# Performance work log

Hardware: AMD Instinct MI355X
Metric: run time of the kernel (lower is better)

## Reference

```python
import jax, jax.numpy as jnp
import numpy as np

B = 4; C_IN = 3; HW = 224
D_MODEL = 384; D_INNER = 768; D_STATE = 16; DT_RANK = 24; D_CONV = 4
N_LAYERS = 4; NUM_CLASSES = 1000
EPS = 1e-5


def setup_inputs() -> dict:
    key = jax.random.key(0)
    ks = jax.random.split(key, 12)
    def rn(k, shape, scale=0.02):
        return jax.random.normal(k, shape, jnp.float32) * scale
    inp = {}
    inp["x"] = jax.random.normal(ks[0], (B, C_IN, HW, HW), jnp.float32)
    inp["patch_w"] = rn(ks[1], (D_MODEL, C_IN, 4, 4))
    inp["patch_b"] = jnp.zeros((D_MODEL,), jnp.float32)
    inp["in_proj_w"] = rn(ks[2], (N_LAYERS, 2 * D_INNER, D_MODEL))
    inp["conv_w"] = rn(ks[3], (N_LAYERS, D_INNER, 1, D_CONV))
    inp["conv_b"] = jnp.zeros((N_LAYERS, D_INNER), jnp.float32)
    inp["x_proj_w"] = rn(ks[4], (N_LAYERS, DT_RANK + 2 * D_STATE, D_INNER))
    inp["dt_proj_w"] = rn(ks[5], (N_LAYERS, D_INNER, DT_RANK))
    inp["dt_proj_b"] = rn(ks[6], (N_LAYERS, D_INNER), 0.1)
    A = jnp.tile(jnp.arange(1, D_STATE + 1, dtype=jnp.float32)[None, :], (D_INNER, 1))
    inp["A_log"] = jnp.tile(jnp.log(A)[None], (N_LAYERS, 1, 1))
    inp["Dp"] = jnp.ones((N_LAYERS, D_INNER), jnp.float32)
    inp["out_proj_w"] = rn(ks[7], (N_LAYERS, D_MODEL, D_INNER))
    inp["norm_w"] = jnp.ones((D_MODEL,), jnp.float32)
    inp["head_w"] = rn(ks[8], (NUM_CLASSES, D_MODEL))
    inp["head_b"] = jnp.zeros((NUM_CLASSES,), jnp.float32)
    return inp


def selective_scan(u, delta, A, Bm, Cm, Dv):
    # u, delta: [b,l,d]; A: [d,n]; Bm, Cm: [b,l,n]; Dv: [d]
    dA = jnp.exp(delta[..., None] * A)                 # [b,l,d,n]
    dBu = (delta * u)[..., None] * Bm[:, :, None, :]   # [b,l,d,n]

    def step(h, inp):
        a, bu, c = inp
        h = a * h + bu                                  # [b,d,n]
        y = jnp.einsum('bdn,bn->bd', h, c)
        return h, y

    h0 = jnp.zeros((u.shape[0], u.shape[2], A.shape[1]), u.dtype)
    xs = (jnp.swapaxes(dA, 0, 1), jnp.swapaxes(dBu, 0, 1), jnp.swapaxes(Cm, 0, 1))
    _, ys = jax.lax.scan(step, h0, xs)                  # ys: [l,b,d]
    y = jnp.swapaxes(ys, 0, 1)                          # [b,l,d]
    return y + u * Dv


def mamba_block(x, p):
    xr = x @ p['in_proj_w'].T                           # [b,l,2*d_inner]
    xc, res = jnp.split(xr, 2, axis=-1)
    # depthwise causal conv1d (left pad d_conv-1 == pad both + truncate right)
    xt = jnp.swapaxes(xc, 1, 2)                         # [b,d_inner,l]
    xt = jax.lax.conv_general_dilated(
        xt, p['conv_w'], (1,), [(D_CONV - 1, 0)],
        feature_group_count=D_INNER,
        dimension_numbers=('NCH', 'OIH', 'NCH')) + p['conv_b'][None, :, None]
    xc = jax.nn.silu(jnp.swapaxes(xt, 1, 2))
    # S6
    dbl = xc @ p['x_proj_w'].T                          # [b,l,dt_rank+2n]
    dt, Bm, Cm = jnp.split(dbl, [DT_RANK, DT_RANK + D_STATE], axis=-1)
    delta = jax.nn.softplus(dt @ p['dt_proj_w'].T + p['dt_proj_b'])
    y = selective_scan(xc, delta, -jnp.exp(p['A_log']), Bm, Cm, p['Dp'])
    y = y * jax.nn.silu(res)
    return y @ p['out_proj_w'].T


def reference(x, patch_w, patch_b, in_proj_w, conv_w, conv_b, x_proj_w,
              dt_proj_w, dt_proj_b, A_log, Dp, out_proj_w, norm_w, head_w, head_b):
    h = jax.lax.conv_general_dilated(
        x, patch_w, (4, 4), 'VALID',
        dimension_numbers=('NCHW', 'OIHW', 'NCHW')) + patch_b[None, :, None, None]
    b, d, hh, ww = h.shape
    t = jnp.transpose(h.reshape(b, d, hh * ww), (0, 2, 1))  # [b,l,d_model]
    layer_params = dict(in_proj_w=in_proj_w, conv_w=conv_w, conv_b=conv_b,
                        x_proj_w=x_proj_w, dt_proj_w=dt_proj_w, dt_proj_b=dt_proj_b,
                        A_log=A_log, Dp=Dp, out_proj_w=out_proj_w)
    for i in range(N_LAYERS):
        p = {k: v[i] for k, v in layer_params.items()}
        t = t + mamba_block(t, p)
    rms = jnp.sqrt(jnp.mean(t * t, axis=-1, keepdims=True) + EPS)
    t = t / rms * norm_w
    pooled = t.mean(axis=1)
    return pooled @ head_w.T + head_b
```

## Files before the change

kernel.cpp:

```cpp
#include <hip/hip_runtime.h>
#include <math.h>


namespace {
constexpr int NB = 4;
constexpr int SL = 3136;
constexpr int DM = 384;
constexpr int DI = 768;
constexpr int DSN = 16;
constexpr int DR = 24;
constexpr int NLAYER = 4;
constexpr int NCLS = 1000;
constexpr int XPN = DR + 2 * DSN;
constexpr int NCHAIN = NB * DI;
constexpr int PTOK = 32;
}

typedef float f32x4 __attribute__((ext_vector_type(4)));
typedef short short8 __attribute__((ext_vector_type(8)));
typedef short short4v __attribute__((ext_vector_type(4)));
typedef unsigned short us4 __attribute__((ext_vector_type(4)));

__device__ __forceinline__ float siluf(float x) { return x / (1.f + expf(-x)); }
__device__ __forceinline__ float softplusf(float x) {
  return fmaxf(x, 0.f) + log1pf(expf(-fabsf(x)));
}
__device__ __forceinline__ unsigned short cvt_bf(float f) {
  unsigned int x = __float_as_uint(f);
  unsigned int r = (x + 0x7fffu + ((x >> 16) & 1u)) >> 16;
  return (unsigned short)r;
}
__device__ __forceinline__ float bf2f(unsigned short v) {
  return __uint_as_float((unsigned int)v << 16);
}

__global__ __launch_bounds__(128) void k_patch(
    const float* __restrict__ x, const float* __restrict__ w,
    const float* __restrict__ bias, float* __restrict__ t,
    unsigned short* __restrict__ tb) {
  __shared__ float patch[PTOK][48];
  const int tid = threadIdx.x;
  const int m0 = blockIdx.x * PTOK;
  const int b = m0 / SL, lbase = m0 % SL;
#pragma unroll
  for (int i = 0; i < 3; ++i) {
    const int c = tid + i * 128;
    const int tok = c / 12, r = c % 12;
    const int ch = r >> 2, kh = r & 3;
    const int l = lbase + tok;
    const int hh = l / 56, ww = l % 56;
    const float4 v =
        *(const float4*)&x[((size_t)(b * 3 + ch) * 224 + (hh * 4 + kh)) * 224 + ww * 4];
    *(float4*)&patch[tok][ch * 16 + kh * 4] = v;
  }
  __syncthreads();
#pragma unroll 1
  for (int i = 0; i < 3; ++i) {
    const int dm = tid + i * 128;
    float4 wr[12];
    const float4* w4 = (const float4*)(w + (size_t)dm * 48);
#pragma unroll
    for (int q = 0; q < 12; ++q) wr[q] = w4[q];
    const float bv = bias[dm];
#pragma unroll 1
    for (int tok0 = 0; tok0 < PTOK; tok0 += 8) {
      float acc[8];
#pragma unroll
      for (int j = 0; j < 8; ++j) acc[j] = bv;
#pragma unroll
      for (int q = 0; q < 12; ++q) {
        const float4 wv = wr[q];
#pragma unroll
        for (int j = 0; j < 8; ++j) {
          const float4 pv = *(const float4*)&patch[tok0 + j][q * 4];
          acc[j] = fmaf(pv.x, wv.x, acc[j]);
          acc[j] = fmaf(pv.y, wv.y, acc[j]);
          acc[j] = fmaf(pv.z, wv.z, acc[j]);
          acc[j] = fmaf(pv.w, wv.w, acc[j]);
        }
      }
#pragma unroll
      for (int j = 0; j < 8; ++j) {
        const size_t o = ((size_t)(m0 + tok0 + j)) * DM + dm;
        t[o] = acc[j];
        tb[o] = cvt_bf(acc[j]);
      }
    }
  }
}

template <int BM, int BN, int MEPI, int NCAP, bool AT>
__global__ __launch_bounds__(256) void k_mgemm(
    const unsigned short* __restrict__ A, const unsigned short* __restrict__ Abf,
    const float* __restrict__ W, float* __restrict__ out,
    float* __restrict__ out2, unsigned short* __restrict__ outb, const int K) {
  constexpr int WM = BM / 2, WN = BN / 2, FM = WM / 16, FN = WN / 16;
  constexpr bool NMASK = (NCAP % BN) != 0;
  __shared__ unsigned short As[BM * 40];
  __shared__ unsigned short Bs[BN * 40];
  const int tid = threadIdx.x;
  const int lane = tid & 63, wave = tid >> 6;
  const int wm = wave >> 1, wn = wave & 1;
  const int m0 = blockIdx.x * BM, n0 = blockIdx.y * BN;
  const int r16 = lane & 15, kg = (lane >> 4) * 8;
  f32x4 acc[FM][FN] = {};
  const int nk = K >> 5;
  for (int kt = 0; kt < nk; ++kt) {
    const int k0 = kt << 5;
    if constexpr (AT) {
#pragma unroll
      for (int it = 0; it < BM / 64; ++it) {
        const int c = tid + 256 * it;
        const int kp = c & 15;
        const int lq = (c >> 4) * 4;
        const int mrow = m0 + lq;
        const int bb = mrow / SL;
        const size_t rowo = (size_t)(bb * K + k0 + 2 * kp) * SL + (mrow - bb * SL);
        const us4 v0 = *(const us4*)&Abf[rowo];
        const us4 v1 = *(const us4*)&Abf[rowo + SL];
#pragma unroll
        for (int e = 0; e < 4; ++e) {
          const unsigned int pk =
              (unsigned int)v0[e] | ((unsigned int)v1[e] << 16);
          *(unsigned int*)&As[(lq + e) * 40 + 2 * kp] = pk;
        }
      }
    } else {
#pragma unroll
      for (int it = 0; it < (BM * 4) / 256; ++it) {
        const int c = tid + 256 * it;
        const int row = c >> 2, ks = (c & 3) * 8;
        *(short8*)&As[row * 40 + ks] =
            *(const short8*)&A[(size_t)(m0 + row) * K + k0 + ks];
      }
    }
#pragma unroll
    for (int it = 0; it < (BN * 8) / 256; ++it) {
      const int c = tid + 256 * it;
      const int row = c >> 3, ks = (c & 7) * 4;
      float4 v = make_float4(0.f, 0.f, 0.f, 0.f);
      if (!NMASK || (n0 + row) < NCAP)
        v = *(const float4*)&W[(size_t)(n0 + row) * K + k0 + ks];
      short4v o4;
      o4[0] = (short)cvt_bf(v.x);
      o4[1] = (short)cvt_bf(v.y);
      o4[2] = (short)cvt_bf(v.z);
      o4[3] = (short)cvt_bf(v.w);
      *(short4v*)&Bs[row * 40 + ks] = o4;
    }
    __syncthreads();
    short8 af[FM], bfv[FN];
#pragma unroll
    for (int i = 0; i < FM; ++i)
      af[i] = *(const short8*)&As[(wm * WM + i * 16 + r16) * 40 + kg];
#pragma unroll
    for (int j = 0; j < FN; ++j)
      bfv[j] = *(const short8*)&Bs[(wn * WN + j * 16 + r16) * 40 + kg];
#pragma unroll
    for (int i = 0; i < FM; ++i)
#pragma unroll
      for (int j = 0; j < FN; ++j)
        acc[i][j] = __builtin_amdgcn_mfma_f32_16x16x32_bf16(af[i], bfv[j],
                                                            acc[i][j], 0, 0, 0);
    __syncthreads();
  }

#pragma unroll
  for (int i = 0; i < FM; ++i) {
#pragma unroll
    for (int j = 0; j < FN; ++j) {
      const int n = n0 + wn * WN + j * 16 + r16;
      const int mb = m0 + wm * WM + i * 16 + ((lane >> 4) << 2);
      f32x4 a = acc[i][j];
      if (MEPI == 0) {
        if (n < DR) {
#pragma unroll
          for (int r = 0; r < 4; ++r) out[(size_t)(mb + r) * DR + n] = a[r];
        } else if (n < NCAP) {
#pragma unroll
          for (int r = 0; r < 4; ++r) out2[(size_t)(mb + r) * 32 + (n - DR)] = a[r];
        }
      } else if (MEPI == 1) {
        unsigned short* base = (unsigned short*)out;
        int nn = n;
        if (n >= DI) { base = (unsigned short*)out2; nn = n - DI; }
        const int bb = mb / SL;
        const int ll = mb - bb * SL;
        us4 o4;
#pragma unroll
        for (int r = 0; r < 4; ++r) o4[r] = cvt_bf(a[r]);
        *(us4*)&base[((size_t)(bb * DI + nn)) * SL + ll] = o4;
      } else {
#pragma unroll
        for (int r = 0; r < 4; ++r) {
          const size_t off = (size_t)(mb + r) * DM + n;
          const float nv = out[off] + a[r];
          out[off] = nv;
          outb[off] = cvt_bf(nv);
        }
      }
    }
  }
}

template <int EPI, bool KTAIL, int NCAP>
__global__ __launch_bounds__(256) void k_gemm(
    const float* __restrict__ A, const float* __restrict__ W,
    const float* __restrict__ bias, float* __restrict__ out, int K, int lda) {
  __shared__ float sm[4352];
  const int tid = threadIdx.x;
  const int m0 = blockIdx.x * 64;
  const int n0 = blockIdx.y * 64;
  const int b = m0 / SL, l0 = m0 % SL;
  const int tm = tid >> 4, tn = tid & 15;
  float acc[4][4] = {};
  float* As = sm;
  float* Ws = sm + 16 * 68;

  const int nk = (K + 15) / 16;
  for (int kt = 0; kt < nk; ++kt) {
    const int k0 = kt * 16;
    {
      const int row = tid >> 2;
      const int kq = (tid & 3) * 4;
      const int kb = k0 + kq;
      float4 v = make_float4(0.f, 0.f, 0.f, 0.f);
      if (!KTAIL || kb < K) v = *(const float4*)&A[(size_t)(m0 + row) * lda + kb];
      As[(kq + 0) * 68 + row] = v.x;
      As[(kq + 1) * 68 + row] = v.y;
      As[(kq + 2) * 68 + row] = v.z;
      As[(kq + 3) * 68 + row] = v.w;
    }
    {
      const int row = tid >> 2;
      const int kq = (tid & 3) * 4;
      const int kb = k0 + kq;
      float4 v = make_float4(0.f, 0.f, 0.f, 0.f);
      const bool nok = (NCAP % 64 == 0) || (n0 + row < NCAP);
      if (nok && (!KTAIL || kb < K)) v = *(const float4*)&W[(size_t)(n0 + row) * K + kb];
      Ws[(kq + 0) * 68 + row] = v.x;
      Ws[(kq + 1) * 68 + row] = v.y;
      Ws[(kq + 2) * 68 + row] = v.z;
      Ws[(kq + 3) * 68 + row] = v.w;
    }
    __syncthreads();
#pragma unroll
    for (int kk = 0; kk < 16; ++kk) {
      const float4 av = *(const float4*)&As[kk * 68 + 4 * tm];
      const float4 wv = *(const float4*)&Ws[kk * 68 + 4 * tn];
      const float ax[4] = {av.x, av.y, av.z, av.w};
      const float wx[4] = {wv.x, wv.y, wv.z, wv.w};
#pragma unroll
      for (int i = 0; i < 4; ++i)
#pragma unroll
        for (int j = 0; j < 4; ++j) acc[i][j] = fmaf(ax[i], wx[j], acc[i][j]);
    }
    __syncthreads();
  }

#pragma unroll
  for (int j = 0; j < 4; ++j) {
    const int nn = 4 * tn + j;
#pragma unroll
    for (int i = 0; i < 4; ++i) {
      float v = acc[i][j];
      if (EPI == 2) v = softplusf(v + bias[n0 + nn]);
      sm[nn * 68 + 4 * tm + i] = v;
    }
  }
  __syncthreads();
  const int row = tid >> 2;
  const int seg = (tid & 3) * 16;
  const float* src = &sm[row * 68 + seg];
  float* dst = out + ((size_t)(b * DI + n0 + row)) * SL + l0 + seg;
#pragma unroll
  for (int q = 0; q < 4; ++q) {
    *(float4*)&dst[q * 4] = *(const float4*)&src[q * 4];
  }
}

__global__ void k_conv(const unsigned short* __restrict__ xcT,
                       const float* __restrict__ cw, const float* __restrict__ cb,
                       unsigned short* __restrict__ uT) {
  const size_t idx = (size_t)blockIdx.x * 256 + threadIdx.x;
  const int l4 = (int)(idx % (SL / 4)) * 4;
  const int bd = (int)(idx / (SL / 4));
  const int d = bd % DI;
  const unsigned short* row = xcT + (size_t)bd * SL;
  const float4 w = *(const float4*)&cw[d * 4];
  const us4 cu = *(const us4*)&row[l4];
  const float c0 = bf2f(cu[0]), c1 = bf2f(cu[1]), c2 = bf2f(cu[2]), c3 = bf2f(cu[3]);
  float p1 = 0.f, p2 = 0.f, p3 = 0.f;
  if (l4 > 0) {
    const us4 pv = *(const us4*)&row[l4 - 4];
    p1 = bf2f(pv[1]); p2 = bf2f(pv[2]); p3 = bf2f(pv[3]);
  }
  const float cbd = cb[d];
  float o0 = cbd + w.w * c0 + w.z * p3 + w.y * p2 + w.x * p1;
  float o1 = cbd + w.w * c1 + w.z * c0 + w.y * p3 + w.x * p2;
  float o2 = cbd + w.w * c2 + w.z * c1 + w.y * c0 + w.x * p3;
  float o3 = cbd + w.w * c3 + w.z * c2 + w.y * c1 + w.x * c0;
  us4 o4;
  o4[0] = cvt_bf(siluf(o0));
  o4[1] = cvt_bf(siluf(o1));
  o4[2] = cvt_bf(siluf(o2));
  o4[3] = cvt_bf(siluf(o3));
  *(us4*)&uT[(size_t)bd * SL + l4] = o4;
}

__global__ __launch_bounds__(256) void k_scanw(
    const float* __restrict__ deltaT, const unsigned short* __restrict__ uT,
    const float* __restrict__ BC, const unsigned short* __restrict__ resT,
    const float* __restrict__ A_log, const float* __restrict__ Dp,
    unsigned short* __restrict__ yT) {
  const int tid = threadIdx.x;
  const int lane = tid & 63, wv = tid >> 6;
  const int n = lane & 15, g = lane >> 4;
  const int chain = blockIdx.x * 4 + wv;
  const int b = chain / DI, d = chain % DI;
  const float a2 = -expf(A_log[d * DSN + n]) * 1.44269504088896341f;
  const float dp = Dp[d];
  const float* drow = deltaT + (size_t)chain * SL;
  const unsigned short* urow = uT + (size_t)chain * SL;
  const unsigned short* resr = resT + (size_t)chain * SL;
  const float* bcb = BC + (size_t)b * SL * 32;
  unsigned short* yr = yT + (size_t)chain * SL;
  float carry = 0.f;
  const bool b0 = n & 1, b1 = (n >> 1) & 1, b2 = (n >> 2) & 1, b3 = (n >> 3) & 1;

  for (int tb = 0; tb < SL; tb += 64) {
    const int l0 = tb + g * 16;
    float da[16], dbu[16];
    float h = 0.f, dsum = 0.f;
#pragma unroll
    for (int k = 0; k < 16; ++k) {
      const float dl = drow[l0 + k];
      const float ul = bf2f(urow[l0 + k]);
      const float Bv = bcb[(size_t)(l0 + k) * 32 + n];
      const float e = exp2f(dl * a2);
      da[k] = e;
      dbu[k] = dl * ul * Bv;
      h = fmaf(e, h, dbu[k]);
      dsum += dl;
    }
    float Aagg = exp2f(a2 * dsum);
    float Bagg = h;
#pragma unroll
    for (int off = 16; off <= 32; off <<= 1) {
      const float Ae = __shfl(Aagg, (lane - off) & 63);
      const float Be = __shfl(Bagg, (lane - off) & 63);
      if (lane >= off) {
        Bagg = fmaf(Aagg, Be, Bagg);
        Aagg *= Ae;
      }
    }
    const float Pa = __shfl(Aagg, (lane - 16) & 63);
    const float Pb = __shfl(Bagg, (lane - 16) & 63);
    const float hstart = (g == 0) ? carry : fmaf(Pa, carry, Pb);
    const float cA = __shfl(Aagg, 48 | n);
    const float cB = __shfl(Bagg, 48 | n);
    float p[16];
    h = hstart;
#pragma unroll
    for (int k = 0; k < 16; ++k) {
      h = fmaf(da[k], h, dbu[k]);
      p[k] = h * bcb[(size_t)(l0 + k) * 32 + 16 + n];
    }
    carry = fmaf(cA, carry, cB);
    float q8[8];
#pragma unroll
    for (int i = 0; i < 8; ++i) {
      const float mine = b0 ? p[2 * i + 1] : p[2 * i];
      const float oth = b0 ? p[2 * i] : p[2 * i + 1];
      q8[i] = mine + __shfl_xor(oth, 1);
    }
    float q4[4];
#pragma unroll
    for (int i = 0; i < 4; ++i) {
      const float mine = b1 ? q8[2 * i + 1] : q8[2 * i];
      const float oth = b1 ? q8[2 * i] : q8[2 * i + 1];
      q4[i] = mine + __shfl_xor(oth, 2);
    }
    float q2[2];
#pragma unroll
    for (int i = 0; i < 2; ++i) {
      const float mine = b2 ? q4[2 * i + 1] : q4[2 * i];
      const float oth = b2 ? q4[2 * i] : q4[2 * i + 1];
      q2[i] = mine + __shfl_xor(oth, 4);
    }
    const float mine = b3 ? q2[1] : q2[0];
    const float oth = b3 ? q2[0] : q2[1];
    const float ysum = mine + __shfl_xor(oth, 8);
    const float uln = bf2f(urow[l0 + n]);
    const float r = bf2f(resr[l0 + n]);
    yr[l0 + n] = cvt_bf((ysum + uln * dp) * siluf(r));
  }
}

__global__ void k_rinv(const float* __restrict__ t, float* __restrict__ rinv) {
  const int row = blockIdx.x;
  const float* tr = t + (size_t)row * DM;
  const int tid = threadIdx.x;
  float ss = 0.f;
#pragma unroll
  for (int k = 0; k < DM / 64; ++k) {
    const float v = tr[tid + k * 64];
    ss = fmaf(v, v, ss);
  }
  ss += __shfl_xor(ss, 1);
  ss += __shfl_xor(ss, 2);
  ss += __shfl_xor(ss, 4);
  ss += __shfl_xor(ss, 8);
  ss += __shfl_xor(ss, 16);
  ss += __shfl_xor(ss, 32);
  if (tid == 0) rinv[row] = 1.f / sqrtf(ss / DM + 1e-5f);
}

__global__ void k_pool(const float* __restrict__ t, const float* __restrict__ rinv,
                       float* __restrict__ part) {
  const int b = blockIdx.x, dmb = blockIdx.y, ch = blockIdx.z;
  const int dm = dmb * 64 + threadIdx.x;
  const int lbeg = ch * (SL / 32);
  float s = 0.f;
  for (int l = lbeg; l < lbeg + SL / 32; ++l)
    s = fmaf(t[((size_t)b * SL + l) * DM + dm], rinv[b * SL + l], s);
  part[((size_t)ch * NB + b) * DM + dm] = s;
}

__global__ void k_head(const float* __restrict__ part, const float* __restrict__ norm_w,
                       const float* __restrict__ hw, const float* __restrict__ hb,
                       float* __restrict__ out) {
  const int b = blockIdx.x;
  const int tid = threadIdx.x;
  __shared__ float pv[DM];
  for (int k = tid; k < DM; k += 64) {
    float s = 0.f;
#pragma unroll
    for (int c = 0; c < 32; ++c) s += part[((size_t)c * NB + b) * DM + k];
    pv[k] = s * norm_w[k] * (1.f / SL);
  }
  __syncthreads();
  const int cls = blockIdx.y * 64 + tid;
  if (cls < NCLS) {
    const float* wr = hw + (size_t)cls * DM;
    float acc = hb[cls];
#pragma unroll 4
    for (int k = 0; k < DM; k += 4) {
      const float4 w4 = *(const float4*)&wr[k];
      acc = fmaf(pv[k], w4.x, acc);
      acc = fmaf(pv[k + 1], w4.y, acc);
      acc = fmaf(pv[k + 2], w4.z, acc);
      acc = fmaf(pv[k + 3], w4.w, acc);
    }
    out[(size_t)b * NCLS + cls] = acc;
  }
}

extern "C" void kernel_launch(void* const* d_in, const int* in_sizes, int n_in,
                              void* d_out, int out_size, void* d_ws, size_t ws_size,
                              hipStream_t stream) {
  (void)in_sizes; (void)n_in; (void)out_size; (void)ws_size;
  const float* x = (const float*)d_in[0];
  const float* patch_w = (const float*)d_in[1];
  const float* patch_b = (const float*)d_in[2];
  const float* in_proj_w = (const float*)d_in[3];
  const float* conv_w = (const float*)d_in[4];
  const float* conv_b = (const float*)d_in[5];
  const float* x_proj_w = (const float*)d_in[6];
  const float* dt_proj_w = (const float*)d_in[7];
  const float* dt_proj_b = (const float*)d_in[8];
  const float* A_log = (const float*)d_in[9];
  const float* Dp = (const float*)d_in[10];
  const float* out_proj_w = (const float*)d_in[11];
  const float* norm_w = (const float*)d_in[12];
  const float* head_w = (const float*)d_in[13];
  const float* head_b = (const float*)d_in[14];

  float* ws = (float*)d_ws;
  size_t o = 0;
  float* t = ws + o;     o += (size_t)NB * SL * DM;
  unsigned short* xcT = (unsigned short*)(ws + o);  o += (size_t)NB * DI * SL / 2;
  unsigned short* resT = (unsigned short*)(ws + o); o += (size_t)NB * DI * SL / 2;
  unsigned short* uT = (unsigned short*)(ws + o);   o += (size_t)NB * DI * SL / 2;
  unsigned short* yT = (unsigned short*)(ws + o);   o += (size_t)NB * DI * SL / 2;
  float* dltT = ws + o;  o += (size_t)NB * DI * SL;
  float* dbl24 = ws + o; o += (size_t)NB * SL * DR;
  float* BC = ws + o;    o += (size_t)NB * SL * 32;
  float* rinv = ws + o;  o += (size_t)NB * SL;
  float* part = ws + o;  o += (size_t)32 * NB * DM;
  unsigned short* tb = (unsigned short*)(ws + o); o += (size_t)NB * SL * DM / 2;

  k_patch<<<(NB * SL) / PTOK, 128, 0, stream>>>(x, patch_w, patch_b, t, tb);

  for (int i = 0; i < NLAYER; ++i) {
    k_mgemm<128, 128, 1, 1536, false><<<dim3(98, 12), 256, 0, stream>>>(
        tb, nullptr, in_proj_w + (size_t)i * 2 * DI * DM, (float*)xcT, (float*)resT,
        nullptr, DM);
    k_conv<<<(NB * DI * SL / 4) / 256, 256, 0, stream>>>(
        xcT, conv_w + (size_t)i * DI * 4, conv_b + (size_t)i * DI, uT);
    k_mgemm<64, 64, 0, XPN, true><<<dim3(196, 1), 256, 0, stream>>>(
        nullptr, uT, x_proj_w + (size_t)i * XPN * DI, dbl24, BC, nullptr, DI);
    k_gemm<2, true, 64><<<dim3(196, 12), 256, 0, stream>>>(
        dbl24, dt_proj_w + (size_t)i * DI * DR, dt_proj_b + (size_t)i * DI, dltT,
        DR, DR);
    k_scanw<<<NCHAIN / 4, 256, 0, stream>>>(
        dltT, uT, BC, resT, A_log + (size_t)i * DI * DSN, Dp + (size_t)i * DI, yT);
    k_mgemm<128, 128, 2, 384, true><<<dim3(98, 3), 256, 0, stream>>>(
        nullptr, yT, out_proj_w + (size_t)i * DM * DI, t, nullptr, tb, DI);
  }

  k_rinv<<<NB * SL, 64, 0, stream>>>(t, rinv);
  k_pool<<<dim3(NB, DM / 64, 32), 64, 0, stream>>>(t, rinv, part);
  k_head<<<dim3(NB, 16), 64, 0, stream>>>(part, norm_w, head_w, head_b, (float*)d_out);
}
```

Measured before the change: 1.137 ms.

## Fuse dt_proj GEMM and softplus into the selective scan kernel

Removes the separate dt_proj GEMM kernel and its fp32 delta buffer of size B×D_INNER×L. Each scan wave now computes delta on the fly: each lane does a 24-wide dot product of the dt-rank row with the per-channel dt weights, applies softplus, and shares the results across the 16-lane group with shuffles. This avoids writing and re-reading a large intermediate and saves one launch per layer. The cost is extra redundant ALU work and reads of dbl24 inside the latency-bound scan.

Result: slower. 1.846 ms (+62.4%).

```diff
diff --git a/kernel.cpp b/kernel.cpp
--- a/kernel.cpp
+++ b/kernel.cpp
@@ -203,82 +203,6 @@
   }
 }
 
-template <int EPI, bool KTAIL, int NCAP>
-__global__ __launch_bounds__(256) void k_gemm(
-    const float* __restrict__ A, const float* __restrict__ W,
-    const float* __restrict__ bias, float* __restrict__ out, int K, int lda) {
-  __shared__ float sm[4352];
-  const int tid = threadIdx.x;
-  const int m0 = blockIdx.x * 64;
-  const int n0 = blockIdx.y * 64;
-  const int b = m0 / SL, l0 = m0 % SL;
-  const int tm = tid >> 4, tn = tid & 15;
-  float acc[4][4] = {};
-  float* As = sm;
-  float* Ws = sm + 16 * 68;
-
-  const int nk = (K + 15) / 16;
-  for (int kt = 0; kt < nk; ++kt) {
-    const int k0 = kt * 16;
-    {
-      const int row = tid >> 2;
-      const int kq = (tid & 3) * 4;
-      const int kb = k0 + kq;
-      float4 v = make_float4(0.f, 0.f, 0.f, 0.f);
-      if (!KTAIL || kb < K) v = *(const float4*)&A[(size_t)(m0 + row) * lda + kb];
-      As[(kq + 0) * 68 + row] = v.x;
-      As[(kq + 1) * 68 + row] = v.y;
-      As[(kq + 2) * 68 + row] = v.z;
-      As[(kq + 3) * 68 + row] = v.w;
-    }
-    {
-      const int row = tid >> 2;
-      const int kq = (tid & 3) * 4;
-      const int kb = k0 + kq;
-      float4 v = make_float4(0.f, 0.f, 0.f, 0.f);
-      const bool nok = (NCAP % 64 == 0) || (n0 + row < NCAP);
-      if (nok && (!KTAIL || kb < K)) v = *(const float4*)&W[(size_t)(n0 + row) * K + kb];
-      Ws[(kq + 0) * 68 + row] = v.x;
-      Ws[(kq + 1) * 68 + row] = v.y;
-      Ws[(kq + 2) * 68 + row] = v.z;
-      Ws[(kq + 3) * 68 + row] = v.w;
-    }
-    __syncthreads();
-#pragma unroll
-    for (int kk = 0; kk < 16; ++kk) {
-      const float4 av = *(const float4*)&As[kk * 68 + 4 * tm];
-      const float4 wv = *(const float4*)&Ws[kk * 68 + 4 * tn];
-      const float ax[4] = {av.x, av.y, av.z, av.w};
-      const float wx[4] = {wv.x, wv.y, wv.z, wv.w};
-#pragma unroll
-      for (int i = 0; i < 4; ++i)
-#pragma unroll
-        for (int j = 0; j < 4; ++j) acc[i][j] = fmaf(ax[i], wx[j], acc[i][j]);
-    }
-    __syncthreads();
-  }
-
-#pragma unroll
-  for (int j = 0; j < 4; ++j) {
-    const int nn = 4 * tn + j;
-#pragma unroll
-    for (int i = 0; i < 4; ++i) {
-      float v = acc[i][j];
-      if (EPI == 2) v = softplusf(v + bias[n0 + nn]);
-      sm[nn * 68 + 4 * tm + i] = v;
-    }
-  }
-  __syncthreads();
-  const int row = tid >> 2;
-  const int seg = (tid & 3) * 16;
-  const float* src = &sm[row * 68 + seg];
-  float* dst = out + ((size_t)(b * DI + n0 + row)) * SL + l0 + seg;
-#pragma unroll
-  for (int q = 0; q < 4; ++q) {
-    *(float4*)&dst[q * 4] = *(const float4*)&src[q * 4];
-  }
-}
-
 __global__ void k_conv(const unsigned short* __restrict__ xcT,
                        const float* __restrict__ cw, const float* __restrict__ cb,
                        unsigned short* __restrict__ uT) {
@@ -309,8 +233,9 @@
 }
 
 __global__ __launch_bounds__(256) void k_scanw(
-    const float* __restrict__ deltaT, const unsigned short* __restrict__ uT,
+    const float* __restrict__ dbl24, const unsigned short* __restrict__ uT,
     const float* __restrict__ BC, const unsigned short* __restrict__ resT,
+    const float* __restrict__ dtw, const float* __restrict__ dtb,
     const float* __restrict__ A_log, const float* __restrict__ Dp,
     unsigned short* __restrict__ yT) {
   const int tid = threadIdx.x;
@@ -320,21 +245,39 @@
   const int b = chain / DI, d = chain % DI;
   const float a2 = -expf(A_log[d * DSN + n]) * 1.44269504088896341f;
   const float dp = Dp[d];
-  const float* drow = deltaT + (size_t)chain * SL;
   const unsigned short* urow = uT + (size_t)chain * SL;
   const unsigned short* resr = resT + (size_t)chain * SL;
   const float* bcb = BC + (size_t)b * SL * 32;
+  const float* dblb = dbl24 + (size_t)b * SL * DR;
   unsigned short* yr = yT + (size_t)chain * SL;
+  float4 dw[6];
+  const float4* dw4 = (const float4*)(dtw + (size_t)d * DR);
+#pragma unroll
+  for (int q = 0; q < 6; ++q) dw[q] = dw4[q];
+  const float dbias = dtb[d];
   float carry = 0.f;
   const bool b0 = n & 1, b1 = (n >> 1) & 1, b2 = (n >> 2) & 1, b3 = (n >> 3) & 1;
 
   for (int tb = 0; tb < SL; tb += 64) {
     const int l0 = tb + g * 16;
+    float dacc = 0.f;
+    {
+      const float4* dr = (const float4*)&dblb[(size_t)(l0 + n) * DR];
+#pragma unroll
+      for (int q = 0; q < 6; ++q) {
+        const float4 v = dr[q];
+        dacc = fmaf(v.x, dw[q].x, dacc);
+        dacc = fmaf(v.y, dw[q].y, dacc);
+        dacc = fmaf(v.z, dw[q].z, dacc);
+        dacc = fmaf(v.w, dw[q].w, dacc);
+      }
+    }
+    const float my_dl = softplusf(dacc + dbias);
     float da[16], dbu[16];
     float h = 0.f, dsum = 0.f;
 #pragma unroll
     for (int k = 0; k < 16; ++k) {
-      const float dl = drow[l0 + k];
+      const float dl = __shfl(my_dl, (lane & 48) | k);
       const float ul = bf2f(urow[l0 + k]);
       const float Bv = bcb[(size_t)(l0 + k) * 32 + n];
       const float e = exp2f(dl * a2);
@@ -483,7 +426,6 @@
   unsigned short* resT = (unsigned short*)(ws + o); o += (size_t)NB * DI * SL / 2;
   unsigned short* uT = (unsigned short*)(ws + o);   o += (size_t)NB * DI * SL / 2;
   unsigned short* yT = (unsigned short*)(ws + o);   o += (size_t)NB * DI * SL / 2;
-  float* dltT = ws + o;  o += (size_t)NB * DI * SL;
   float* dbl24 = ws + o; o += (size_t)NB * SL * DR;
   float* BC = ws + o;    o += (size_t)NB * SL * 32;
   float* rinv = ws + o;  o += (size_t)NB * SL;
@@ -500,11 +442,10 @@
         xcT, conv_w + (size_t)i * DI * 4, conv_b + (size_t)i * DI, uT);
     k_mgemm<64, 64, 0, XPN, true><<<dim3(196, 1), 256, 0, stream>>>(
         nullptr, uT, x_proj_w + (size_t)i * XPN * DI, dbl24, BC, nullptr, DI);
-    k_gemm<2, true, 64><<<dim3(196, 12), 256, 0, stream>>>(
-        dbl24, dt_proj_w + (size_t)i * DI * DR, dt_proj_b + (size_t)i * DI, dltT,
-        DR, DR);
     k_scanw<<<NCHAIN / 4, 256, 0, stream>>>(
-        dltT, uT, BC, resT, A_log + (size_t)i * DI * DSN, Dp + (size_t)i * DI, yT);
+        dbl24, uT, BC, resT, dt_proj_w + (size_t)i * DI * DR,
+        dt_proj_b + (size_t)i * DI, A_log + (size_t)i * DI * DSN,
+        Dp + (size_t)i * DI, yT);
     k_mgemm<128, 128, 2, 384, true><<<dim3(98, 3), 256, 0, stream>>>(
         nullptr, yT, out_proj_w + (size_t)i * DM * DI, t, nullptr, tb, DI);
   }
```
